# Kernel optimization log

Hardware: AMD Instinct MI355X
Metric: run time of the kernel (lower is better)

The kernel has to match this reference:

```python
import jax, jax.numpy as jnp
import numpy as np

N = 50000
E = 800000
IN_DIM, HID, OUT = 128, 256, 256


def setup_inputs() -> dict:
    key = jax.random.key(0)
    ks = jax.random.split(key, 6)
    x = jax.random.normal(ks[0], (N, IN_DIM), dtype=jnp.float32)
    edge_index = jax.random.randint(ks[1], (2, E), 0, N, dtype=jnp.int64)
    W1 = jax.random.normal(ks[2], (IN_DIM, HID), dtype=jnp.float32) / np.sqrt(IN_DIM)
    b1 = jnp.zeros((HID,), dtype=jnp.float32)
    W2 = jax.random.normal(ks[3], (HID, OUT), dtype=jnp.float32) / np.sqrt(HID)
    b2 = jnp.zeros((OUT,), dtype=jnp.float32)
    return {"x": x, "edge_index": edge_index, "W1": W1, "b1": b1, "W2": W2, "b2": b2}


def _gcn_conv(x, edge_index, W, b):
    """PyG GCNConv: add self-loops, symmetric deg^-1/2 norm, linear, scatter-add, bias."""
    n = x.shape[0]
    loops = jnp.arange(n, dtype=edge_index.dtype)
    src = jnp.concatenate([edge_index[0], loops])  # [E+N]
    dst = jnp.concatenate([edge_index[1], loops])  # [E+N]
    deg = jax.ops.segment_sum(jnp.ones(src.shape[0], dtype=x.dtype), dst, num_segments=n)
    dinv = jnp.where(deg > 0, jax.lax.rsqrt(deg), jnp.zeros_like(deg))
    norm = dinv[src] * dinv[dst]  # [E+N]
    h = x @ W  # [N, out] small GEMM before gather (PyG order)
    msg = h[src] * norm[:, None]  # [E+N, out] -- dominant memory traffic
    out = jax.ops.segment_sum(msg, dst, num_segments=n)
    return out + b


def reference(x, edge_index, W1, b1, W2, b2):
    h = jax.nn.relu(_gcn_conv(x, edge_index, W1, b1))
    # dropout is identity in eval mode
    out = _gcn_conv(h, edge_index, W2, b2)
    # F.normalize(p=2, dim=-1, eps=1e-12)
    nrm = jnp.maximum(jnp.linalg.norm(out, axis=-1, keepdims=True), 1e-12)
    return out / nrm
```

## Files before the change

### kernel.cpp

```cpp
#include <hip/hip_runtime.h>
#include <hip/hip_bf16.h>


#define NNODE 50000
#define FDIM 256
#define SCAN_CHUNK 2048
#define CAST_BLOCKS 3125
#define WCONV_BLOCKS 48

typedef __attribute__((ext_vector_type(8))) short short8;
typedef __attribute__((ext_vector_type(4))) float f32x4;

__device__ __forceinline__ float bflo(unsigned int u) {
    union { unsigned int i; float f; } c;
    c.i = u << 16;
    return c.f;
}
__device__ __forceinline__ float bfhi(unsigned int u) {
    union { unsigned int i; float f; } c;
    c.i = u & 0xFFFF0000u;
    return c.f;
}
__device__ __forceinline__ unsigned short f2bf(float f) {
    __hip_bfloat16 h = __float2bfloat16(f);
    return *reinterpret_cast<unsigned short*>(&h);
}
__device__ __forceinline__ unsigned int pk(float lo, float hi) {
    return (unsigned int)f2bf(lo) | ((unsigned int)f2bf(hi) << 16);
}

__global__ __launch_bounds__(256) void prep_kernel(
    const float* __restrict__ x, unsigned int* __restrict__ xb,
    const float* __restrict__ W1, unsigned short* __restrict__ Wf1,
    const float* __restrict__ W2, unsigned short* __restrict__ Wf2,
    const int* __restrict__ ei, int* __restrict__ counts, int E) {
    int b = blockIdx.x, t = threadIdx.x;
    if (b < CAST_BLOCKS) {
        int i = b * 256 + t;
        const float4* xf = reinterpret_cast<const float4*>(x);
        float4 p = xf[2 * i], q = xf[2 * i + 1];
        uint4 o;
        o.x = pk(p.x, p.y); o.y = pk(p.z, p.w);
        o.z = pk(q.x, q.y); o.w = pk(q.z, q.w);
        reinterpret_cast<uint4*>(xb)[i] = o;
    } else if (b < CAST_BLOCKS + WCONV_BLOCKS) {
        int idx = (b - CAST_BLOCKS) * 256 + t;
        const float* W;
        unsigned short* Wf;
        bool perm;
        if (idx < 16 * 256) { W = W1; Wf = Wf1; perm = false; }
        else { idx -= 16 * 256; W = W2; Wf = Wf2; perm = true; }
        int g = idx >> 8, c = idx & 255;
        unsigned short vals[8];
#pragma unroll
        for (int j = 0; j < 8; ++j) {
            int k = 8 * g + j;
            int f = perm ? ((k & ~63) | ((k & 3) << 4) | ((k >> 2) & 15)) : k;
            vals[j] = f2bf(W[(size_t)f * 256 + c]);
        }
        *reinterpret_cast<ushort4*>(&Wf[(size_t)idx * 8]) =
            make_ushort4(vals[0], vals[1], vals[2], vals[3]);
        *reinterpret_cast<ushort4*>(&Wf[(size_t)idx * 8 + 4]) =
            make_ushort4(vals[4], vals[5], vals[6], vals[7]);
    } else {
        int e = (b - CAST_BLOCKS - WCONV_BLOCKS) * 256 + t;
        if (e < E) atomicAdd(&counts[ei[E + e]], 1);
    }
}

__global__ __launch_bounds__(256) void scan_part1(const int* __restrict__ counts,
                                                  int* __restrict__ bsum, int n) {
    __shared__ int ws[4];
    int b = blockIdx.x, t = threadIdx.x;
    int base = b * SCAN_CHUNK + t * 8;
    int s = 0;
#pragma unroll
    for (int j = 0; j < 8; ++j) {
        int i = base + j;
        if (i < n) s += counts[i];
    }
#pragma unroll
    for (int off = 32; off >= 1; off >>= 1) s += __shfl_xor(s, off, 64);
    if ((t & 63) == 0) ws[t >> 6] = s;
    __syncthreads();
    if (t == 0) bsum[b] = ws[0] + ws[1] + ws[2] + ws[3];
}

__global__ __launch_bounds__(256) void scan_part3(const int* __restrict__ counts,
                                                  const int* __restrict__ bsum,
                                                  int* __restrict__ row_ptr,
                                                  int* __restrict__ cursor,
                                                  float* __restrict__ dinv,
                                                  int n, int nb) {
    __shared__ int ws[4];
    __shared__ int s_boff, s_total;
    int b = blockIdx.x, t = threadIdx.x, lane = t & 63, wid = t >> 6;
    if (t < 64) {
        int v = (t < nb) ? bsum[t] : 0;
        int incl = v;
#pragma unroll
        for (int off = 1; off < 64; off <<= 1) {
            int u = __shfl_up(incl, off, 64);
            if (t >= off) incl += u;
        }
        if (t == b) s_boff = incl - v;
        if (t == nb - 1) s_total = incl;
    }
    __syncthreads();
    if (b == 0 && t == 0) row_ptr[n] = s_total;

    int base = b * SCAN_CHUNK + t * 8;
    int v[8];
    int s = 0;
#pragma unroll
    for (int j = 0; j < 8; ++j) {
        int i = base + j;
        v[j] = (i < n) ? counts[i] : 0;
        s += v[j];
    }
    int incl = s;
#pragma unroll
    for (int off = 1; off < 64; off <<= 1) {
        int u = __shfl_up(incl, off, 64);
        if (lane >= off) incl += u;
    }
    if (lane == 63) ws[wid] = incl;
    __syncthreads();
    int woff = 0;
    for (int u = 0; u < wid; ++u) woff += ws[u];
    int ex = s_boff + woff + incl - s;
#pragma unroll
    for (int j = 0; j < 8; ++j) {
        int i = base + j;
        if (i < n) {
            row_ptr[i] = ex;
            cursor[i] = ex;
            dinv[i] = rsqrtf((float)(v[j] + 1));
        }
        ex += v[j];
    }
}

__global__ void fill_kernel(const int* __restrict__ ei, const float* __restrict__ dinv,
                            int* __restrict__ cursor, int2* __restrict__ edata, int E) {
    int e = blockIdx.x * blockDim.x + threadIdx.x;
    if (e < E) {
        int s = ei[e];
        int d = ei[E + e];
        int pos = atomicAdd(&cursor[d], 1);
        float nm = dinv[s] * dinv[d];
        edata[pos] = make_int2(s, __float_as_int(nm));
    }
}

__global__ __launch_bounds__(256) void agg1_kernel(const unsigned int* __restrict__ xb,
                                                   const int* __restrict__ rowp,
                                                   const int2* __restrict__ edata,
                                                   const float* __restrict__ dinv,
                                                   unsigned int* __restrict__ A1, int n) {
    int node = (blockIdx.x * blockDim.x + threadIdx.x) >> 6;
    int lane = threadIdx.x & 63;
    if (node >= n) return;
    float di = dinv[node];
    float d2 = di * di;
    unsigned int sv = xb[(size_t)node * 64 + lane];
    float a0 = bflo(sv) * d2, a1 = bfhi(sv) * d2;
    int beg = rowp[node], end = rowp[node + 1];
#pragma unroll 4
    for (int e = beg; e < end; ++e) {
        int2 ed = edata[e];
        float nm = __int_as_float(ed.y);
        unsigned int v = xb[(size_t)ed.x * 64 + lane];
        a0 = fmaf(bflo(v), nm, a0);
        a1 = fmaf(bfhi(v), nm, a1);
    }
    A1[(size_t)node * 64 + lane] = pk(a0, a1);
}

__global__ __launch_bounds__(256) void agg2_kernel(const uint2* __restrict__ hb,
                                                   const int* __restrict__ rowp,
                                                   const int2* __restrict__ edata,
                                                   const float* __restrict__ dinv,
                                                   uint2* __restrict__ A2, int n) {
    int node = (blockIdx.x * blockDim.x + threadIdx.x) >> 6;
    int lane = threadIdx.x & 63;
    if (node >= n) return;
    float di = dinv[node];
    float d2 = di * di;
    uint2 sv = hb[(size_t)node * 64 + lane];
    float a0 = bflo(sv.x) * d2, a1 = bfhi(sv.x) * d2;
    float a2 = bflo(sv.y) * d2, a3 = bfhi(sv.y) * d2;
    int beg = rowp[node], end = rowp[node + 1];
#pragma unroll 4
    for (int e = beg; e < end; ++e) {
        int2 ed = edata[e];
        float nm = __int_as_float(ed.y);
        uint2 v = hb[(size_t)ed.x * 64 + lane];
        a0 = fmaf(bflo(v.x), nm, a0);
        a1 = fmaf(bfhi(v.x), nm, a1);
        a2 = fmaf(bflo(v.y), nm, a2);
        a3 = fmaf(bfhi(v.y), nm, a3);
    }
    uint2 o;
    o.x = pk(a0, a1);
    o.y = pk(a2, a3);
    A2[(size_t)node * 64 + lane] = o;
}

template <int K, int EPI>
__global__ __launch_bounds__(512) void gemm_fused(const unsigned short* __restrict__ A,
                                                  const unsigned short* __restrict__ Wf,
                                                  const float* __restrict__ bias,
                                                  void* __restrict__ outp, int n) {
    __shared__ unsigned short As[128 * K];
    __shared__ __align__(16) float ssred[128][4];
    int t = threadIdx.x;
    int row0 = blockIdx.x * 128;

#pragma unroll
    for (int i = 0; i < (128 * K) / (8 * 512); ++i) {
        int o = 8 * (t + 512 * i);
        int row = o / K, k = o % K;
        int srow = row0 + row;
        uint4 v = make_uint4(0u, 0u, 0u, 0u);
        if (srow < n) v = *reinterpret_cast<const uint4*>(&A[(size_t)srow * K + k]);
        int gx = (k >> 3) ^ (row & 7);
        *reinterpret_cast<uint4*>(&As[row * K + gx * 8]) = v;
    }
    __syncthreads();

    int lane = t & 63, wv = t >> 6;
    int rw = wv >> 2, cw = wv & 3;
    int l15 = lane & 15, lhi = lane >> 4;
    f32x4 zero = {0.f, 0.f, 0.f, 0.f};
    f32x4 acc[4][4];
#pragma unroll
    for (int rf = 0; rf < 4; ++rf)
#pragma unroll
        for (int cf = 0; cf < 4; ++cf) acc[rf][cf] = zero;

#pragma unroll
    for (int s = 0; s < K / 32; ++s) {
        int g = 4 * s + lhi;
        short8 a[4], b[4];
#pragma unroll
        for (int rf = 0; rf < 4; ++rf) {
            int row = 64 * rw + 16 * rf + l15;
            a[rf] = *reinterpret_cast<const short8*>(&As[row * K + (g ^ (row & 7)) * 8]);
        }
#pragma unroll
        for (int cf = 0; cf < 4; ++cf) {
            int c = 64 * cw + 16 * cf + l15;
            b[cf] = *reinterpret_cast<const short8*>(&Wf[((size_t)g * 256 + c) * 8]);
        }
#pragma unroll
        for (int rf = 0; rf < 4; ++rf)
#pragma unroll
            for (int cf = 0; cf < 4; ++cf)
                acc[rf][cf] = __builtin_amdgcn_mfma_f32_16x16x32_bf16(a[rf], b[cf], acc[rf][cf], 0, 0, 0);
    }

    if constexpr (EPI == 0) {
        unsigned short* H = (unsigned short*)outp;
        float bv[4];
#pragma unroll
        for (int cf = 0; cf < 4; ++cf) bv[cf] = bias[64 * cw + 16 * cf + l15];
#pragma unroll
        for (int rf = 0; rf < 4; ++rf) {
#pragma unroll
            for (int j = 0; j < 4; ++j) {
                int row = row0 + 64 * rw + 16 * rf + 4 * lhi + j;
                if (row < n) {
                    float c0 = fmaxf(acc[rf][0][j] + bv[0], 0.f);
                    float c1 = fmaxf(acc[rf][1][j] + bv[1], 0.f);
                    float c2 = fmaxf(acc[rf][2][j] + bv[2], 0.f);
                    float c3 = fmaxf(acc[rf][3][j] + bv[3], 0.f);
                    uint2 o;
                    o.x = pk(c0, c1);
                    o.y = pk(c2, c3);
                    *reinterpret_cast<uint2*>(&H[(size_t)row * 256 + 64 * cw + 4 * l15]) = o;
                }
            }
        }
    } else {
        float* O = (float*)outp;
        float ss[4][4];
#pragma unroll
        for (int rf = 0; rf < 4; ++rf)
#pragma unroll
            for (int j = 0; j < 4; ++j) ss[rf][j] = 0.f;
#pragma unroll
        for (int cf = 0; cf < 4; ++cf) {
            int col = 64 * cw + 16 * cf + l15;
            float bc = bias[col];
#pragma unroll
            for (int rf = 0; rf < 4; ++rf)
#pragma unroll
                for (int j = 0; j < 4; ++j) {
                    float v = acc[rf][cf][j] + bc;
                    acc[rf][cf][j] = v;
                    ss[rf][j] = fmaf(v, v, ss[rf][j]);
                }
        }
#pragma unroll
        for (int rf = 0; rf < 4; ++rf)
#pragma unroll
            for (int j = 0; j < 4; ++j) {
#pragma unroll
                for (int off = 1; off <= 8; off <<= 1)
                    ss[rf][j] += __shfl_xor(ss[rf][j], off, 64);
            }
        if (l15 == 0) {
#pragma unroll
            for (int rf = 0; rf < 4; ++rf)
#pragma unroll
                for (int j = 0; j < 4; ++j)
                    ssred[64 * rw + 16 * rf + 4 * lhi + j][cw] = ss[rf][j];
        }
        __syncthreads();
        float rinv[4][4];
#pragma unroll
        for (int rf = 0; rf < 4; ++rf)
#pragma unroll
            for (int j = 0; j < 4; ++j) {
                float4 s4 = *reinterpret_cast<const float4*>(
                    ssred[64 * rw + 16 * rf + 4 * lhi + j]);
                float tot = s4.x + s4.y + s4.z + s4.w;
                rinv[rf][j] = 1.f / fmaxf(sqrtf(tot), 1e-12f);
            }
#pragma unroll
        for (int cf = 0; cf < 4; ++cf) {
            int col = 64 * cw + 16 * cf + l15;
#pragma unroll
            for (int rf = 0; rf < 4; ++rf)
#pragma unroll
                for (int j = 0; j < 4; ++j) {
                    int row = row0 + 64 * rw + 16 * rf + 4 * lhi + j;
                    if (row < n)
                        __builtin_nontemporal_store(acc[rf][cf][j] * rinv[rf][j],
                                                    &O[(size_t)row * 256 + col]);
                }
        }
    }
}

extern "C" void kernel_launch(void* const* d_in, const int* in_sizes, int n_in,
                              void* d_out, int out_size, void* d_ws, size_t ws_size,
                              hipStream_t stream) {
    const float* x  = (const float*)d_in[0];
    const int*   ei = (const int*)d_in[1];
    const float* W1 = (const float*)d_in[2];
    const float* b1 = (const float*)d_in[3];
    const float* W2 = (const float*)d_in[4];
    const float* b2 = (const float*)d_in[5];
    float* out = (float*)d_out;

    const int N = NNODE;
    const int E = in_sizes[1] / 2;
    const int NB = (N + SCAN_CHUNK - 1) / SCAN_CHUNK;

    char* ws = (char*)d_ws;
    size_t off = 0;
    auto alloc = [&](size_t bytes) -> void* {
        void* p = ws + off;
        off = (off + bytes + 255) & ~(size_t)255;
        return p;
    };
    unsigned int*   xb  = (unsigned int*)alloc((size_t)N * 128 * 2);
    unsigned int*   A1  = (unsigned int*)alloc((size_t)N * 128 * 2);
    unsigned short* Bbf = (unsigned short*)alloc((size_t)N * FDIM * 2);
    uint2*          A2  = (uint2*)alloc((size_t)N * FDIM * 2);
    unsigned short* Wf1 = (unsigned short*)alloc((size_t)16 * 256 * 8 * 2);
    unsigned short* Wf2 = (unsigned short*)alloc((size_t)32 * 256 * 8 * 2);
    int*   counts = (int*)alloc((size_t)N * 4);
    int*   rowp   = (int*)alloc((size_t)(N + 1) * 4);
    int*   cursor = (int*)alloc((size_t)N * 4);
    float* dinv   = (float*)alloc((size_t)N * 4);
    int2*  edata  = (int2*)alloc((size_t)E * 8);
    int*   bsum   = (int*)alloc((size_t)NB * 4);

    hipMemsetAsync(counts, 0, (size_t)N * 4, stream);
    int count_blocks = (E + 255) / 256;
    prep_kernel<<<CAST_BLOCKS + WCONV_BLOCKS + count_blocks, 256, 0, stream>>>(
        x, xb, W1, Wf1, W2, Wf2, ei, counts, E);
    scan_part1<<<NB, 256, 0, stream>>>(counts, bsum, N);
    scan_part3<<<NB, 256, 0, stream>>>(counts, bsum, rowp, cursor, dinv, N, NB);
    fill_kernel<<<(E + 255) / 256, 256, 0, stream>>>(ei, dinv, cursor, edata, E);

    agg1_kernel<<<(N * 64 + 255) / 256, 256, 0, stream>>>(xb, rowp, edata, dinv, A1, N);
    gemm_fused<128, 0><<<(N + 127) / 128, 512, 0, stream>>>(
        (const unsigned short*)A1, Wf1, b1, Bbf, N);
    agg2_kernel<<<(N * 64 + 255) / 256, 256, 0, stream>>>(
        (const uint2*)Bbf, rowp, edata, dinv, A2, N);
    gemm_fused<256, 1><<<(N + 127) / 128, 512, 0, stream>>>(
        (const unsigned short*)A2, Wf2, b2, out, N);
}
```

Measured before the change: 240.0 us.

## Bucket CSR edges by source-range phase to improve gather locality

Each destination's edge list is split into 13 buckets keyed on the source index's high bits (s>>12), so within a row the edges are sorted coarsely by source. Neighbor gathers in the aggregation kernels then touch source rows in increasing address ranges, which is meant to improve L2 locality. In exchange the count, rowptr and cursor arrays grow 13x, the scan needs an extra multi-block offset kernel, and a separate dinv kernel is added. That adds launch and scan overhead for arrays of about 650k entries.

```diff
diff --git a/kernel.cpp b/kernel.cpp
--- a/kernel.cpp
+++ b/kernel.cpp
@@ -4,6 +4,9 @@
 
 #define NNODE 50000
 #define FDIM 256
+#define NPH 13
+#define PHSH 12
+#define NCNT (NNODE * NPH)
 #define SCAN_CHUNK 2048
 #define CAST_BLOCKS 3125
 #define WCONV_BLOCKS 48
@@ -64,12 +67,16 @@
             make_ushort4(vals[4], vals[5], vals[6], vals[7]);
     } else {
         int e = (b - CAST_BLOCKS - WCONV_BLOCKS) * 256 + t;
-        if (e < E) atomicAdd(&counts[ei[E + e]], 1);
+        if (e < E) {
+            int s = ei[e];
+            int d = ei[E + e];
+            atomicAdd(&counts[d * NPH + (s >> PHSH)], 1);
+        }
     }
 }
 
 __global__ __launch_bounds__(256) void scan_part1(const int* __restrict__ counts,
-                                                  int* __restrict__ bsum, int n) {
+                                                  int* __restrict__ bsum, int m) {
     __shared__ int ws[4];
     int b = blockIdx.x, t = threadIdx.x;
     int base = b * SCAN_CHUNK + t * 8;
@@ -77,7 +84,7 @@
 #pragma unroll
     for (int j = 0; j < 8; ++j) {
         int i = base + j;
-        if (i < n) s += counts[i];
+        if (i < m) s += counts[i];
     }
 #pragma unroll
     for (int off = 32; off >= 1; off >>= 1) s += __shfl_xor(s, off, 64);
@@ -86,36 +93,38 @@
     if (t == 0) bsum[b] = ws[0] + ws[1] + ws[2] + ws[3];
 }
 
-__global__ __launch_bounds__(256) void scan_part3(const int* __restrict__ counts,
-                                                  const int* __restrict__ bsum,
-                                                  int* __restrict__ row_ptr,
-                                                  int* __restrict__ cursor,
-                                                  float* __restrict__ dinv,
-                                                  int n, int nb) {
-    __shared__ int ws[4];
-    __shared__ int s_boff, s_total;
-    int b = blockIdx.x, t = threadIdx.x, lane = t & 63, wid = t >> 6;
-    if (t < 64) {
-        int v = (t < nb) ? bsum[t] : 0;
+__global__ void scan_part2(const int* __restrict__ bsum, int* __restrict__ boff,
+                           int* __restrict__ row_ptr, int nb, int m) {
+    int l = threadIdx.x;
+    int carry = 0;
+    for (int base = 0; base < nb; base += 64) {
+        int i = base + l;
+        int v = (i < nb) ? bsum[i] : 0;
         int incl = v;
 #pragma unroll
         for (int off = 1; off < 64; off <<= 1) {
             int u = __shfl_up(incl, off, 64);
-            if (t >= off) incl += u;
-        }
-        if (t == b) s_boff = incl - v;
-        if (t == nb - 1) s_total = incl;
-    }
-    __syncthreads();
-    if (b == 0 && t == 0) row_ptr[n] = s_total;
-
+            if (l >= off) incl += u;
+        }
+        if (i < nb) boff[i] = carry + incl - v;
+        carry += __shfl(incl, 63, 64);
+    }
+    if (l == 0) row_ptr[m] = carry;
+}
+
+__global__ __launch_bounds__(256) void scan_part3(const int* __restrict__ counts,
+                                                  const int* __restrict__ boff,
+                                                  int* __restrict__ row_ptr,
+                                                  int* __restrict__ cursor, int m) {
+    __shared__ int ws[4];
+    int b = blockIdx.x, t = threadIdx.x, lane = t & 63, wid = t >> 6;
     int base = b * SCAN_CHUNK + t * 8;
     int v[8];
     int s = 0;
 #pragma unroll
     for (int j = 0; j < 8; ++j) {
         int i = base + j;
-        v[j] = (i < n) ? counts[i] : 0;
+        v[j] = (i < m) ? counts[i] : 0;
         s += v[j];
     }
     int incl = s;
@@ -128,16 +137,20 @@
     __syncthreads();
     int woff = 0;
     for (int u = 0; u < wid; ++u) woff += ws[u];
-    int ex = s_boff + woff + incl - s;
+    int ex = boff[b] + woff + incl - s;
 #pragma unroll
     for (int j = 0; j < 8; ++j) {
         int i = base + j;
-        if (i < n) {
-            row_ptr[i] = ex;
-            cursor[i] = ex;
-            dinv[i] = rsqrtf((float)(v[j] + 1));
-        }
+        if (i < m) { row_ptr[i] = ex; cursor[i] = ex; }
         ex += v[j];
+    }
+}
+
+__global__ void dinv_kernel(const int* __restrict__ rowp, float* __restrict__ dinv, int n) {
+    int i = blockIdx.x * blockDim.x + threadIdx.x;
+    if (i < n) {
+        int deg = rowp[(i + 1) * NPH] - rowp[i * NPH];
+        dinv[i] = rsqrtf((float)(deg + 1));
     }
 }
 
@@ -147,7 +160,7 @@
     if (e < E) {
         int s = ei[e];
         int d = ei[E + e];
-        int pos = atomicAdd(&cursor[d], 1);
+        int pos = atomicAdd(&cursor[d * NPH + (s >> PHSH)], 1);
         float nm = dinv[s] * dinv[d];
         edata[pos] = make_int2(s, __float_as_int(nm));
     }
@@ -165,7 +178,7 @@
     float d2 = di * di;
     unsigned int sv = xb[(size_t)node * 64 + lane];
     float a0 = bflo(sv) * d2, a1 = bfhi(sv) * d2;
-    int beg = rowp[node], end = rowp[node + 1];
+    int beg = rowp[node * NPH], end = rowp[node * NPH + NPH];
 #pragma unroll 4
     for (int e = beg; e < end; ++e) {
         int2 ed = edata[e];
@@ -190,7 +203,7 @@
     uint2 sv = hb[(size_t)node * 64 + lane];
     float a0 = bflo(sv.x) * d2, a1 = bfhi(sv.x) * d2;
     float a2 = bflo(sv.y) * d2, a3 = bfhi(sv.y) * d2;
-    int beg = rowp[node], end = rowp[node + 1];
+    int beg = rowp[node * NPH], end = rowp[node * NPH + NPH];
 #pragma unroll 4
     for (int e = beg; e < end; ++e) {
         int2 ed = edata[e];
@@ -357,7 +370,8 @@
 
     const int N = NNODE;
     const int E = in_sizes[1] / 2;
-    const int NB = (N + SCAN_CHUNK - 1) / SCAN_CHUNK;
+    const int M = NCNT;
+    const int NB = (M + SCAN_CHUNK - 1) / SCAN_CHUNK;
 
     char* ws = (char*)d_ws;
     size_t off = 0;
@@ -372,19 +386,22 @@
     uint2*          A2  = (uint2*)alloc((size_t)N * FDIM * 2);
     unsigned short* Wf1 = (unsigned short*)alloc((size_t)16 * 256 * 8 * 2);
     unsigned short* Wf2 = (unsigned short*)alloc((size_t)32 * 256 * 8 * 2);
-    int*   counts = (int*)alloc((size_t)N * 4);
-    int*   rowp   = (int*)alloc((size_t)(N + 1) * 4);
-    int*   cursor = (int*)alloc((size_t)N * 4);
+    int*   counts = (int*)alloc((size_t)M * 4);
+    int*   rowp   = (int*)alloc((size_t)(M + 1) * 4);
+    int*   cursor = (int*)alloc((size_t)M * 4);
     float* dinv   = (float*)alloc((size_t)N * 4);
     int2*  edata  = (int2*)alloc((size_t)E * 8);
     int*   bsum   = (int*)alloc((size_t)NB * 4);
-
-    hipMemsetAsync(counts, 0, (size_t)N * 4, stream);
+    int*   boff   = (int*)alloc((size_t)NB * 4);
+
+    hipMemsetAsync(counts, 0, (size_t)M * 4, stream);
     int count_blocks = (E + 255) / 256;
     prep_kernel<<<CAST_BLOCKS + WCONV_BLOCKS + count_blocks, 256, 0, stream>>>(
         x, xb, W1, Wf1, W2, Wf2, ei, counts, E);
-    scan_part1<<<NB, 256, 0, stream>>>(counts, bsum, N);
-    scan_part3<<<NB, 256, 0, stream>>>(counts, bsum, rowp, cursor, dinv, N, NB);
+    scan_part1<<<NB, 256, 0, stream>>>(counts, bsum, M);
+    scan_part2<<<1, 64, 0, stream>>>(bsum, boff, rowp, NB, M);
+    scan_part3<<<NB, 256, 0, stream>>>(counts, boff, rowp, cursor, M);
+    dinv_kernel<<<(N + 255) / 256, 256, 0, stream>>>(rowp, dinv, N);
     fill_kernel<<<(E + 255) / 256, 256, 0, stream>>>(ei, dinv, cursor, edata, E);
 
     agg1_kernel<<<(N * 64 + 255) / 256, 256, 0, stream>>>(xb, rowp, edata, dinv, A1, N);
```

Result: no change. 237.2 us, median of 2 (-1.2%).
